# Performance work log

Hardware: AMD Instinct MI355X
Metric: run time of the kernel (lower is better)

The kernel has to match this reference:

```python
import jax, jax.numpy as jnp
import numpy as np

B, D_IN, H, NZ, NC = 32768, 768, 2048, 128, 1024
EPS, NITERS = 0.5, 15


def setup_inputs() -> dict:
    key = jax.random.key(0)
    ks = jax.random.split(key, 4)
    x = jax.random.normal(ks[0], (B, D_IN), jnp.float32)
    # scaled init so feature magnitudes keep exp(-dist/eps) in f32 range
    W1 = jax.random.normal(ks[1], (D_IN, H), jnp.float32) / np.sqrt(D_IN)
    b1 = jnp.zeros((H,), jnp.float32)
    W2 = jax.random.normal(ks[2], (H, NZ), jnp.float32) / np.sqrt(H)
    b2 = jnp.zeros((NZ,), jnp.float32)
    centroids = jax.random.normal(ks[3], (NC, NZ), jnp.float32)
    return {
        'x': x, 'W1': W1, 'b1': b1, 'W2': W2, 'b2': b2,
        'centroids': centroids,
        'cluster_counts': jnp.zeros((NC,), jnp.int32),
        'raw_counts': jnp.zeros((NC,), jnp.int32),
        'total_soft_counts': jnp.zeros((NC,), jnp.float32),
    }


def _sinkhorn(scores, eps=EPS, niters=NITERS):
    # scores: [B, K].  Q: [K, B], matches torch reference where sum(Q) = col-sums.
    Q = jnp.exp(scores / eps).T
    Q = Q / jnp.sum(Q, axis=0, keepdims=True)
    K, Bb = Q.shape
    r = 1.0 / K
    c = 1.0 / Bb

    def body(Q, _):
        Q = Q * (r / jnp.sum(Q, axis=1))[:, None]
        Q = Q * (c / jnp.sum(Q, axis=0))[None, :]
        return Q, None

    Q, _ = jax.lax.scan(body, Q, None, length=niters)
    return (Q / jnp.sum(Q, axis=0, keepdims=True)).T  # [B, K]


def reference(x, W1, b1, W2, b2, centroids, cluster_counts, raw_counts, total_soft_counts):
    # fc backbone: Linear -> ReLU -> Linear
    fv = jax.nn.relu(x @ W1 + b1) @ W2 + b2                        # [B, nz]
    # pairwise euclidean distances to centroids (cdist via gram trick;
    # avoids materializing the [B, nc, nz] broadcast torch creates)
    sq = (jnp.sum(fv * fv, axis=1)[:, None]
          + jnp.sum(centroids * centroids, axis=1)[None, :]
          - 2.0 * fv @ centroids.T)
    cluster_dists = jnp.sqrt(jnp.maximum(sq, 1e-12))               # [B, nc]

    # sinkhorn branch (no_grad in torch)
    soft_assignments = jax.lax.stop_gradient(_sinkhorn(-cluster_dists))
    batch_assignments = jnp.argmin(soft_assignments, axis=1)       # [B]
    soft_counts = jnp.sum(soft_assignments, axis=0)                # [nc]
    # soft_train=False: gather assigned distances
    loss = jnp.mean(jnp.take_along_axis(cluster_dists, batch_assignments[:, None], axis=1))

    # scatter-accumulate counts
    new_raw = raw_counts.at[jnp.argmin(cluster_dists, axis=1)].add(1)
    new_cluster = cluster_counts.at[batch_assignments].add(1)
    new_total_soft = total_soft_counts + soft_counts
    return loss, batch_assignments, soft_counts, new_raw, new_cluster, new_total_soft
```

## Files before the change

### kernel.cpp

```cpp
#include <hip/hip_runtime.h>
#include <math.h>

#define BN    32768
#define DIN   768
#define HN    2048
#define NZ    128
#define NCN   1024

typedef __attribute__((ext_vector_type(8))) short s16x8;
typedef __attribute__((ext_vector_type(4))) float f32x4;
typedef unsigned short u16;

#define MFMA16(a,b,c) __builtin_amdgcn_mfma_f32_16x16x32_bf16(a,b,c,0,0,0)

__device__ __forceinline__ u16 bf16_rne(float x){
  unsigned u = __float_as_uint(x);
  unsigned r = (u + 0x7FFFu + ((u >> 16) & 1u)) >> 16;
  return (u16)r;
}
__device__ __forceinline__ float bf16_tof(u16 h){
  return __uint_as_float(((unsigned)h) << 16);
}
__device__ __forceinline__ void split3(float x, u16& h, u16& m, u16& l){
  h = bf16_rne(x);
  float r1 = x - bf16_tof(h);
  m = bf16_rne(r1);
  float r2 = r1 - bf16_tof(m);
  l = bf16_rne(r2);
}

__device__ __forceinline__ void gload16(const void* gsrc, void* lds){
  __builtin_amdgcn_global_load_lds(
      (const __attribute__((address_space(1))) unsigned int*)gsrc,
      (__attribute__((address_space(3))) unsigned int*)lds, 16, 0, 0);
}

__global__ __launch_bounds__(1024) void k0_init(float* u, int* hraw, int* hclu){
  const int k = threadIdx.x;
  u[k] = 1.0f;
  hraw[k] = 0;
  hclu[k] = 0;
}

__global__ __launch_bounds__(256) void c_split(
    const float* __restrict__ in, u16* __restrict__ oh, u16* __restrict__ om,
    u16* __restrict__ ol, int n4)
{
  const int i = blockIdx.x*256 + threadIdx.x;
  if (i >= n4) return;
  const f32x4 v = *(const f32x4*)&in[(size_t)i*4];
  ushort4 h4, m4, l4;
  split3(v[0], h4.x, m4.x, l4.x);
  split3(v[1], h4.y, m4.y, l4.y);
  split3(v[2], h4.z, m4.z, l4.z);
  split3(v[3], h4.w, m4.w, l4.w);
  *(ushort4*)&oh[(size_t)i*4] = h4;
  *(ushort4*)&om[(size_t)i*4] = m4;
  *(ushort4*)&ol[(size_t)i*4] = l4;
}

__global__ __launch_bounds__(256) void c_tsplit(
    const float* __restrict__ in, int R, int C,
    u16* __restrict__ oh, u16* __restrict__ om, u16* __restrict__ ol)
{
  __shared__ float L[64][65];
  const int t = threadIdx.x;
  const int bi = blockIdx.x, bj = blockIdx.y;
  #pragma unroll
  for (int m=0;m<4;++m){
    int flat = t + 256*m;
    int r = flat >> 4, c4 = (flat & 15) << 2;
    const float4 v = *(const float4*)&in[(size_t)(bi*64 + r)*C + bj*64 + c4];
    L[r][c4+0] = v.x; L[r][c4+1] = v.y; L[r][c4+2] = v.z; L[r][c4+3] = v.w;
  }
  __syncthreads();
  #pragma unroll
  for (int m=0;m<4;++m){
    int flat = t + 256*m;
    int oc = flat >> 4, k4 = (flat & 15) << 2;
    ushort4 h4, m4, l4;
    split3(L[k4+0][oc], h4.x, m4.x, l4.x);
    split3(L[k4+1][oc], h4.y, m4.y, l4.y);
    split3(L[k4+2][oc], h4.z, m4.z, l4.z);
    split3(L[k4+3][oc], h4.w, m4.w, l4.w);
    size_t off = (size_t)(bj*64 + oc)*R + bi*64 + k4;
    *(ushort4*)&oh[off] = h4;
    *(ushort4*)&om[off] = m4;
    *(ushort4*)&ol[off] = l4;
  }
}

__global__ __launch_bounds__(256) void c_norm(
    const float* __restrict__ in, float* __restrict__ out)
{
  const int w = threadIdx.x >> 6, l = threadIdx.x & 63;
  const int row = blockIdx.x*4 + w;
  const float2 v = *(const float2*)&in[(size_t)row*128 + l*2];
  float s = v.x*v.x + v.y*v.y;
  #pragma unroll
  for (int off=32; off; off>>=1) s += __shfl_xor(s, off, 64);
  if (l == 0) out[row] = s;
}

__global__ __launch_bounds__(256, 2) void k1_mfma(
    const u16* __restrict__ Xh, const u16* __restrict__ Xm, const u16* __restrict__ Xl,
    const u16* __restrict__ W1h, const u16* __restrict__ W1m, const u16* __restrict__ W1l,
    const float* __restrict__ b1,
    const u16* __restrict__ W2h, const u16* __restrict__ W2m, const u16* __restrict__ W2l,
    const float* __restrict__ b2, float* __restrict__ fv)
{
  __shared__ __align__(16) unsigned char sm[73728];
  unsigned char* xsr = sm;
  unsigned char* wsr = sm + 24576;

  const int t  = threadIdx.x;
  const int l  = t & 63;
  const int wn = t >> 6;
  const int g  = (l >> 4) & 3;
  const int lr = l & 15;
  const int row0 = blockIdx.x * 64;

  f32x4 fvacc[4][2];
  #pragma unroll
  for (int mf=0;mf<4;++mf){
    fvacc[mf][0] = (f32x4){0.f,0.f,0.f,0.f};
    fvacc[mf][1] = (f32x4){0.f,0.f,0.f,0.f};
  }

  #pragma unroll 1
  for (int g0 = 0; g0 < 8; ++g0){
    f32x4 a1acc[4][4];
    #pragma unroll
    for (int mf=0;mf<4;++mf)
      #pragma unroll
      for (int j=0;j<4;++j) a1acc[mf][j] = (f32x4){0.f,0.f,0.f,0.f};

    #pragma unroll 1
    for (int ks = 0; ks < 12; ++ks){
      #pragma unroll
      for (int i=0;i<6;++i){
        const int ci = wn*6 + i;
        const int s  = ci >> 3;
        const int rb = ci & 7;
        const int xr = rb*8 + (l >> 3);
        const int q  = l & 7;
        const u16* Xp = (s==0) ? Xh : ((s==1) ? Xm : Xl);
        const u16* src = Xp + (size_t)(row0 + xr)*768 + ks*64 + ((q ^ (xr & 7)) << 3);
        gload16(src, xsr + s*8192 + rb*1024);
      }
      #pragma unroll
      for (int sub2=0; sub2<2; ++sub2){
        #pragma unroll
        for (int i=0;i<12;++i){
          const int ci = wn*12 + i;
          const int s  = ci >> 4;
          const int rb = ci & 15;
          const int rloc = rb*8 + (l >> 3);
          const int q  = l & 7;
          const u16* Wp = (s==0) ? W1h : ((s==1) ? W1m : W1l);
          const u16* src = Wp + (size_t)(g0*256 + sub2*128 + rloc)*768 + ks*64
                              + ((q ^ (rloc & 7)) << 3);
          gload16(src, wsr + s*16384 + rb*1024);
        }
        __syncthreads();

        #pragma unroll
        for (int kk=0;kk<2;++kk){
          s16x8 Bf[3][2], Af[3][4];
          #pragma unroll
          for (int s=0;s<3;++s){
            #pragma unroll
            for (int nf=0;nf<2;++nf){
              const int br = wn*32 + nf*16 + lr;
              Bf[s][nf] = *(const s16x8*)(wsr + s*16384 + br*128 + ((16*(g + 4*kk)) ^ ((br & 7) << 4)));
            }
            #pragma unroll
            for (int mf=0;mf<4;++mf){
              const int ar = mf*16 + lr;
              Af[s][mf] = *(const s16x8*)(xsr + s*8192 + ar*128 + ((16*(g + 4*kk)) ^ ((ar & 7) << 4)));
            }
          }
          #pragma unroll
          for (int mf=0;mf<4;++mf){
            #pragma unroll
            for (int nf=0;nf<2;++nf){
              f32x4 acc = a1acc[mf][sub2*2+nf];
              acc = MFMA16(Af[0][mf], Bf[0][nf], acc);
              acc = MFMA16(Af[0][mf], Bf[1][nf], acc);
              acc = MFMA16(Af[1][mf], Bf[0][nf], acc);
              acc = MFMA16(Af[1][mf], Bf[1][nf], acc);
              acc = MFMA16(Af[0][mf], Bf[2][nf], acc);
              acc = MFMA16(Af[2][mf], Bf[0][nf], acc);
              a1acc[mf][sub2*2+nf] = acc;
            }
          }
        }
        __syncthreads();
      }
    }

    float b1v[2][2];
    #pragma unroll
    for (int s2=0;s2<2;++s2)
      #pragma unroll
      for (int nf=0;nf<2;++nf)
        b1v[s2][nf] = b1[g0*256 + s2*128 + wn*32 + nf*16 + lr];

    #pragma unroll
    for (int h=0; h<4; ++h){
      #pragma unroll
      for (int i=0;i<12;++i){
        const int ci = wn*12 + i;
        const int s  = ci >> 4;
        const int rb = ci & 15;
        const int rloc = rb*8 + (l >> 3);
        const int q  = l & 7;
        const u16* Wp = (s==0) ? W2h : ((s==1) ? W2m : W2l);
        const u16* src = Wp + (size_t)rloc*2048 + g0*256 + h*64 + ((q ^ (rloc & 7)) << 3);
        gload16(src, wsr + s*16384 + rb*1024);
      }
      if ((wn >> 1) == (h & 1)){
        #pragma unroll
        for (int mf=0;mf<4;++mf){
          #pragma unroll
          for (int nf=0;nf<2;++nf){
            const int klocal = (wn & 1)*32 + nf*16 + lr;
            #pragma unroll
            for (int r=0;r<4;++r){
              float vv = a1acc[mf][(h>>1)*2+nf][r] + b1v[h>>1][nf];
              vv = vv > 0.f ? vv : 0.f;
              u16 sh, sm2, sl;
              split3(vv, sh, sm2, sl);
              const int ar = mf*16 + g*4 + r;
              const int bo = ar*128 + ((2*klocal) ^ ((ar & 7) << 4));
              *(u16*)(xsr + bo)         = sh;
              *(u16*)(xsr + 8192 + bo)  = sm2;
              *(u16*)(xsr + 16384 + bo) = sl;
            }
          }
        }
      }
      __syncthreads();

      #pragma unroll
      for (int kk=0;kk<2;++kk){
        s16x8 Bf[3][2], Af[3][4];
        #pragma unroll
        for (int s=0;s<3;++s){
          #pragma unroll
          for (int nf=0;nf<2;++nf){
            const int br = wn*32 + nf*16 + lr;
            Bf[s][nf] = *(const s16x8*)(wsr + s*16384 + br*128 + ((16*(g + 4*kk)) ^ ((br & 7) << 4)));
          }
          #pragma unroll
          for (int mf=0;mf<4;++mf){
            const int ar = mf*16 + lr;
            Af[s][mf] = *(const s16x8*)(xsr + s*8192 + ar*128 + ((16*(g + 4*kk)) ^ ((ar & 7) << 4)));
          }
        }
        #pragma unroll
        for (int mf=0;mf<4;++mf){
          #pragma unroll
          for (int nf=0;nf<2;++nf){
            f32x4 acc = fvacc[mf][nf];
            acc = MFMA16(Af[0][mf], Bf[0][nf], acc);
            acc = MFMA16(Af[0][mf], Bf[1][nf], acc);
            acc = MFMA16(Af[1][mf], Bf[0][nf], acc);
            acc = MFMA16(Af[1][mf], Bf[1][nf], acc);
            acc = MFMA16(Af[0][mf], Bf[2][nf], acc);
            acc = MFMA16(Af[2][mf], Bf[0][nf], acc);
            fvacc[mf][nf] = acc;
          }
        }
      }
      __syncthreads();
    }
  }

  const float b2v0 = b2[wn*32 + lr];
  const float b2v1 = b2[wn*32 + 16 + lr];
  #pragma unroll
  for (int mf=0;mf<4;++mf){
    #pragma unroll
    for (int nf=0;nf<2;++nf){
      #pragma unroll
      for (int r=0;r<4;++r){
        const int frow = row0 + mf*16 + g*4 + r;
        const int col  = wn*32 + nf*16 + lr;
        fv[(size_t)frow*NZ + col] = fvacc[mf][nf][r] + ((nf==0) ? b2v0 : b2v1);
      }
    }
  }
}

__global__ __launch_bounds__(256, 2) void k2_mfma(
    const u16* __restrict__ fvh, const u16* __restrict__ fvm, const u16* __restrict__ fvl,
    const u16* __restrict__ ch,  const u16* __restrict__ cm,  const u16* __restrict__ cl,
    const float* __restrict__ fvn, const float* __restrict__ cn,
    float* __restrict__ Q0)
{
  __shared__ __align__(16) unsigned char bs[49152];
  __shared__ float cnl[NCN];
  const int t  = threadIdx.x;
  const int l  = t & 63;
  const int wn = t >> 6;
  const int g  = (l >> 4) & 3;
  const int lr = l & 15;
  const int row0 = blockIdx.x * 64;
  const int arow = row0 + wn*16 + lr;

  s16x8 Af[3][4];
  #pragma unroll
  for (int kk=0;kk<4;++kk){
    const size_t ao = (size_t)arow*128 + kk*32 + g*8;
    Af[0][kk] = *(const s16x8*)&fvh[ao];
    Af[1][kk] = *(const s16x8*)&fvm[ao];
    Af[2][kk] = *(const s16x8*)&fvl[ao];
  }
  #pragma unroll
  for (int m=0;m<4;++m) cnl[t + 256*m] = cn[t + 256*m];
  const f32x4 fvnv = *(const f32x4*)&fvn[row0 + wn*16 + g*4];

  #pragma unroll 1
  for (int cc = 0; cc < NCN; cc += 64){
    #pragma unroll
    for (int i=0;i<12;++i){
      const int ci = wn*12 + i;
      const int s  = ci >> 4;
      const int rb = ci & 15;
      const int crow = rb*4 + (l >> 4);
      const int q  = l & 15;
      const u16* Cp = (s==0) ? ch : ((s==1) ? cm : cl);
      const u16* src = Cp + (size_t)(cc + crow)*128 + ((q ^ (crow & 15)) << 3);
      gload16(src, bs + s*16384 + rb*1024);
    }
    __syncthreads();

    f32x4 acc[4];
    #pragma unroll
    for (int nf=0;nf<4;++nf) acc[nf] = (f32x4){0.f,0.f,0.f,0.f};

    #pragma unroll
    for (int kk=0;kk<4;++kk){
      s16x8 Bq[3][4];
      #pragma unroll
      for (int nf=0;nf<4;++nf){
        const int br = nf*16 + lr;
        const int base = br*256 + (((g + 4*kk) ^ (br & 15)) << 4);
        Bq[0][nf] = *(const s16x8*)(bs + base);
        Bq[1][nf] = *(const s16x8*)(bs + 16384 + base);
        Bq[2][nf] = *(const s16x8*)(bs + 32768 + base);
      }
      #pragma unroll
      for (int nf=0;nf<4;++nf){
        f32x4 a = acc[nf];
        a = MFMA16(Af[0][kk], Bq[0][nf], a);
        a = MFMA16(Af[0][kk], Bq[1][nf], a);
        a = MFMA16(Af[1][kk], Bq[0][nf], a);
        a = MFMA16(Af[1][kk], Bq[1][nf], a);
        a = MFMA16(Af[0][kk], Bq[2][nf], a);
        a = MFMA16(Af[2][kk], Bq[0][nf], a);
        acc[nf] = a;
      }
    }

    #pragma unroll
    for (int nf=0;nf<4;++nf){
      const int n = cc + nf*16 + lr;
      const float cv = cnl[n];
      #pragma unroll
      for (int r=0;r<4;++r){
        float sq = fvnv[r] + cv - 2.0f*acc[nf][r];
        sq = sq > 1e-12f ? sq : 1e-12f;
        const float d = sqrtf(sq);
        Q0[(size_t)(row0 + wn*16 + g*4 + r)*NCN + n] = expf(-2.0f*d);
      }
    }
    __syncthreads();
  }
}

__global__ __launch_bounds__(256) void k3_pass(
    const float* __restrict__ Q0, const float* __restrict__ u,
    float* __restrict__ S_part, float alpha)
{
  __shared__ __align__(16) float Sw[4][NCN];
  const int t = threadIdx.x;
  const int w = t >> 6, l = t & 63;

  f32x4 uu[4], sacc[4];
  #pragma unroll
  for (int j=0;j<4;++j){
    uu[j] = *(const f32x4*)&u[4*(l + 64*j)];
    sacc[j] = (f32x4){0.f,0.f,0.f,0.f};
  }

  const int gw = blockIdx.x*4 + w;
  const size_t b0 = (size_t)gw * 32;
  for (int rr=0; rr<32; ++rr){
    const f32x4* qrow = (const f32x4*)(Q0 + (b0 + rr)*NCN);
    f32x4 q4[4];
    float part = 0.f;
    #pragma unroll
    for (int j=0;j<4;++j){
      q4[j] = qrow[l + 64*j];
      part += q4[j][0]*uu[j][0]; part += q4[j][1]*uu[j][1];
      part += q4[j][2]*uu[j][2]; part += q4[j][3]*uu[j][3];
    }
    #pragma unroll
    for (int off=32; off; off>>=1) part += __shfl_xor(part, off, 64);
    const float v = alpha / part;
    #pragma unroll
    for (int j=0;j<4;++j){
      sacc[j][0] += q4[j][0]*v; sacc[j][1] += q4[j][1]*v;
      sacc[j][2] += q4[j][2]*v; sacc[j][3] += q4[j][3]*v;
    }
  }
  #pragma unroll
  for (int j=0;j<4;++j) *(f32x4*)&Sw[w][4*(l + 64*j)] = sacc[j];
  __syncthreads();
  #pragma unroll
  for (int m=0;m<4;++m){
    int k = t + 256*m;
    S_part[(size_t)blockIdx.x*NCN + k] = ((Sw[0][k]+Sw[1][k])+(Sw[2][k]+Sw[3][k]));
  }
}

__global__ __launch_bounds__(256) void k4_unew(
    const float* __restrict__ S_part, float* __restrict__ u)
{
  __shared__ float P[4][64];
  const int t = threadIdx.x;
  const int col = blockIdx.x*64 + (t & 63);
  const int s4 = t >> 6;
  float p = 0.f;
  for (int i=0;i<64;++i)
    p += S_part[(size_t)(s4*64 + i)*NCN + col];
  P[s4][t & 63] = p;
  __syncthreads();
  if (s4 == 0){
    float tot = ((P[0][t] + P[1][t]) + (P[2][t] + P[3][t]));
    u[col] = (1.0f/1024.0f) / tot;
  }
}

__device__ __forceinline__ float compv(const f32x4 v, int c){
  return (c==0)?v[0]:(c==1)?v[1]:(c==2)?v[2]:v[3];
}

__global__ __launch_bounds__(256) void k5_final(
    const float* __restrict__ Q0, const float* __restrict__ u,
    float* __restrict__ softc_part, float* __restrict__ loss_part,
    int* __restrict__ hist_raw, int* __restrict__ hist_clu,
    float* __restrict__ out_ba)
{
  __shared__ __align__(16) float Sw[4][NCN];
  __shared__ float lossw[4];
  const int t = threadIdx.x;
  const int w = t >> 6, l = t & 63;

  f32x4 uu[4], sacc[4];
  #pragma unroll
  for (int j=0;j<4;++j){
    uu[j] = *(const f32x4*)&u[4*(l + 64*j)];
    sacc[j] = (f32x4){0.f,0.f,0.f,0.f};
  }

  const int gw = blockIdx.x*4 + w;
  const size_t b0 = (size_t)gw * 32;
  float lacc = 0.f;
  for (int rr=0; rr<32; ++rr){
    const size_t b = b0 + rr;
    const f32x4* qrow = (const f32x4*)(Q0 + b*NCN);
    f32x4 q4[4], wv4[4];
    float part = 0.f;
    #pragma unroll
    for (int j=0;j<4;++j){
      q4[j] = qrow[l + 64*j];
      wv4[j][0] = uu[j][0]*q4[j][0]; wv4[j][1] = uu[j][1]*q4[j][1];
      wv4[j][2] = uu[j][2]*q4[j][2]; wv4[j][3] = uu[j][3]*q4[j][3];
      part += wv4[j][0]; part += wv4[j][1]; part += wv4[j][2]; part += wv4[j][3];
    }
    #pragma unroll
    for (int off=32; off; off>>=1) part += __shfl_xor(part, off, 64);
    const float inv = 1.0f / part;

    float smin = wv4[0][0] * inv; int kmin = 4*l; float qat = q4[0][0];
    float qmax = q4[0][0];        int kmax = 4*l;
    #pragma unroll
    for (int j=0;j<4;++j){
      #pragma unroll
      for (int c=0;c<4;++c){
        if (j==0 && c==0) continue;
        float qv = compv(q4[j], c);
        float sv = compv(wv4[j], c) * inv;
        int k = 4*l + 256*j + c;
        if (sv < smin){ smin = sv; kmin = k; qat = qv; }
        if (qv > qmax){ qmax = qv; kmax = k; }
      }
    }
    #pragma unroll
    for (int off=32; off; off>>=1){
      float s2 = __shfl_xor(smin, off, 64);
      int   k2 = __shfl_xor(kmin, off, 64);
      float q2 = __shfl_xor(qat,  off, 64);
      if (s2 < smin || (s2 == smin && k2 < kmin)){ smin=s2; kmin=k2; qat=q2; }
      float m2 = __shfl_xor(qmax, off, 64);
      int   i2 = __shfl_xor(kmax, off, 64);
      if (m2 > qmax || (m2 == qmax && i2 < kmax)){ qmax=m2; kmax=i2; }
    }
    #pragma unroll
    for (int j=0;j<4;++j){
      sacc[j][0] += wv4[j][0]*inv; sacc[j][1] += wv4[j][1]*inv;
      sacc[j][2] += wv4[j][2]*inv; sacc[j][3] += wv4[j][3]*inv;
    }
    if (l == 0){
      out_ba[b] = (float)kmin;
      atomicAdd(&hist_clu[kmin], 1);
      atomicAdd(&hist_raw[kmax], 1);
      lacc += -0.5f * logf(qat);
    }
  }
  #pragma unroll
  for (int j=0;j<4;++j) *(f32x4*)&Sw[w][4*(l + 64*j)] = sacc[j];
  if (l == 0) lossw[w] = lacc;
  __syncthreads();
  #pragma unroll
  for (int m=0;m<4;++m){
    int k = t + 256*m;
    softc_part[(size_t)blockIdx.x*NCN + k] = ((Sw[0][k]+Sw[1][k])+(Sw[2][k]+Sw[3][k]));
  }
  if (t == 0) loss_part[blockIdx.x] = ((lossw[0]+lossw[1])+(lossw[2]+lossw[3]));
}

__global__ __launch_bounds__(1024) void k6_fin(
    const float* __restrict__ softc_part, const float* __restrict__ loss_part,
    const int* __restrict__ hist_raw, const int* __restrict__ hist_clu,
    const int* __restrict__ raw_in, const int* __restrict__ clu_in,
    const float* __restrict__ tsoft_in, float* __restrict__ out)
{
  const int k = threadIdx.x;
  float s0=0.f,s1=0.f,s2=0.f,s3=0.f;
  for (int blk=0; blk<256; blk+=4){
    s0 += softc_part[(size_t)(blk+0)*NCN + k];
    s1 += softc_part[(size_t)(blk+1)*NCN + k];
    s2 += softc_part[(size_t)(blk+2)*NCN + k];
    s3 += softc_part[(size_t)(blk+3)*NCN + k];
  }
  const float s = ((s0+s1)+(s2+s3));
  out[1 + BN + k]           = s;
  out[1 + BN + NCN + k]     = (float)(raw_in[k] + hist_raw[k]);
  out[1 + BN + 2*NCN + k]   = (float)(clu_in[k] + hist_clu[k]);
  out[1 + BN + 3*NCN + k]   = tsoft_in[k] + s;
  if (k == 0){
    float ls = 0.f;
    for (int i=0;i<256;++i) ls += loss_part[i];
    out[0] = ls / 32768.0f;
  }
}

extern "C" void kernel_launch(void* const* d_in, const int* in_sizes, int n_in,
                              void* d_out, int out_size, void* d_ws, size_t ws_size,
                              hipStream_t stream) {
  (void)in_sizes; (void)n_in; (void)out_size; (void)ws_size;
  const float* x      = (const float*)d_in[0];
  const float* W1     = (const float*)d_in[1];
  const float* b1     = (const float*)d_in[2];
  const float* W2     = (const float*)d_in[3];
  const float* b2     = (const float*)d_in[4];
  const float* cent   = (const float*)d_in[5];
  const int*   clu_in = (const int*)d_in[6];
  const int*   raw_in = (const int*)d_in[7];
  const float* tsoft  = (const float*)d_in[8];
  float* out = (float*)d_out;

  float* ws        = (float*)d_ws;
  float* fv        = ws;
  float* Q0        = ws + 4194304;
  u16*   Xh        = (u16*)Q0;
  u16*   Xm        = Xh + 25165824;
  u16*   Xl        = Xm + 25165824;
  float* u         = ws + 41943040;
  float* S_part    = u + 1024;
  float* softc_par = S_part + 524288;
  float* loss_par  = softc_par + 262144;
  int*   hist_raw  = (int*)(loss_par + 256);
  int*   hist_clu  = hist_raw + 1024;
  float* wbase     = (float*)(hist_clu + 1024);
  u16* W1Th = (u16*)wbase;
  u16* W1Tm = W1Th + 1572864;
  u16* W1Tl = W1Tm + 1572864;
  u16* W2Th = W1Tl + 1572864;
  u16* W2Tm = W2Th + 262144;
  u16* W2Tl = W2Tm + 262144;
  u16* fvh = (u16*)wbase;
  u16* fvm = fvh + 4194304;
  u16* fvl = fvm + 4194304;
  u16* ch  = fvl + 4194304;
  u16* cm  = ch  + 131072;
  u16* cl  = cm  + 131072;
  float* fvn = wbase + 6488064;
  float* cn  = fvn + 32768;

  c_split <<<24576, 256, 0, stream>>>(x, Xh, Xm, Xl, 6291456);
  c_tsplit<<<dim3(12, 32), 256, 0, stream>>>(W1, 768, 2048, W1Th, W1Tm, W1Tl);
  c_tsplit<<<dim3(32, 2),  256, 0, stream>>>(W2, 2048, 128, W2Th, W2Tm, W2Tl);
  k0_init<<<1, 1024, 0, stream>>>(u, hist_raw, hist_clu);

  k1_mfma<<<512, 256, 0, stream>>>(Xh, Xm, Xl, W1Th, W1Tm, W1Tl, b1,
                                   W2Th, W2Tm, W2Tl, b2, fv);

  c_split<<<4096, 256, 0, stream>>>(fv,   fvh, fvm, fvl, 1048576);
  c_split<<<128,  256, 0, stream>>>(cent, ch,  cm,  cl,  32768);
  c_norm <<<8192, 256, 0, stream>>>(fv,   fvn);
  c_norm <<<256,  256, 0, stream>>>(cent, cn);

  k2_mfma<<<512, 256, 0, stream>>>(fvh, fvm, fvl, ch, cm, cl, fvn, cn, Q0);

  for (int it = 0; it < 15; ++it){
    const float alpha = (it == 0) ? 1.0f : (1.0f/32768.0f);
    k3_pass<<<256, 256, 0, stream>>>(Q0, u, S_part, alpha);
    k4_unew<<<16, 256, 0, stream>>>(S_part, u);
  }
  k5_final<<<256, 256, 0, stream>>>(Q0, u, softc_par, loss_par,
                                    hist_raw, hist_clu, out + 1);
  k6_fin<<<1, 1024, 0, stream>>>(softc_par, loss_par, hist_raw, hist_clu,
                                 raw_in, clu_in, tsoft, out);
}
```

Before: 1.454 ms.

## Restructure fused MLP chunking, swizzle blocks, and widen Sinkhorn pass grids

The fused MLP kernel now processes the hidden dimension in 128-wide chunks instead of 256, halving the first-layer accumulator registers, and it issues the W2 tile load after the ReLU/split write. Block indices in k1 and k2 are swizzled so that neighbouring blocks handle spread-out rows. The Sinkhorn row pass and the final kernel launch twice as many blocks with 16 rows per wave, and the row pass batches four rows so their shuffle reductions interleave. The column-reduction kernel uses 64 blocks with a tree reduction, and the workspace layout is moved to hold the larger partial-sum arrays. The aim is more parallelism and occupancy in the memory-bound Sinkhorn loop and lower register pressure in the GEMM, in exchange for more partial sums to reduce and more W1 re-streaming.

```diff
diff --git a/kernel.cpp b/kernel.cpp
--- a/kernel.cpp
+++ b/kernel.cpp
@@ -118,7 +118,9 @@
   const int wn = t >> 6;
   const int g  = (l >> 4) & 3;
   const int lr = l & 15;
-  const int row0 = blockIdx.x * 64;
+  const int bid = blockIdx.x;
+  const int swz = (bid & 7)*64 + (bid >> 3);
+  const int row0 = swz * 64;
 
   f32x4 fvacc[4][2];
   #pragma unroll
@@ -128,12 +130,13 @@
   }
 
   #pragma unroll 1
-  for (int g0 = 0; g0 < 8; ++g0){
-    f32x4 a1acc[4][4];
-    #pragma unroll
-    for (int mf=0;mf<4;++mf)
-      #pragma unroll
-      for (int j=0;j<4;++j) a1acc[mf][j] = (f32x4){0.f,0.f,0.f,0.f};
+  for (int nc = 0; nc < 16; ++nc){
+    f32x4 a1acc[4][2];
+    #pragma unroll
+    for (int mf=0;mf<4;++mf){
+      a1acc[mf][0] = (f32x4){0.f,0.f,0.f,0.f};
+      a1acc[mf][1] = (f32x4){0.f,0.f,0.f,0.f};
+    }
 
     #pragma unroll 1
     for (int ks = 0; ks < 12; ++ks){
@@ -149,77 +152,58 @@
         gload16(src, xsr + s*8192 + rb*1024);
       }
       #pragma unroll
-      for (int sub2=0; sub2<2; ++sub2){
-        #pragma unroll
-        for (int i=0;i<12;++i){
-          const int ci = wn*12 + i;
-          const int s  = ci >> 4;
-          const int rb = ci & 15;
-          const int rloc = rb*8 + (l >> 3);
-          const int q  = l & 7;
-          const u16* Wp = (s==0) ? W1h : ((s==1) ? W1m : W1l);
-          const u16* src = Wp + (size_t)(g0*256 + sub2*128 + rloc)*768 + ks*64
-                              + ((q ^ (rloc & 7)) << 3);
-          gload16(src, wsr + s*16384 + rb*1024);
-        }
-        __syncthreads();
-
-        #pragma unroll
-        for (int kk=0;kk<2;++kk){
-          s16x8 Bf[3][2], Af[3][4];
-          #pragma unroll
-          for (int s=0;s<3;++s){
-            #pragma unroll
-            for (int nf=0;nf<2;++nf){
-              const int br = wn*32 + nf*16 + lr;
-              Bf[s][nf] = *(const s16x8*)(wsr + s*16384 + br*128 + ((16*(g + 4*kk)) ^ ((br & 7) << 4)));
-            }
-            #pragma unroll
-            for (int mf=0;mf<4;++mf){
-              const int ar = mf*16 + lr;
-              Af[s][mf] = *(const s16x8*)(xsr + s*8192 + ar*128 + ((16*(g + 4*kk)) ^ ((ar & 7) << 4)));
-            }
-          }
-          #pragma unroll
-          for (int mf=0;mf<4;++mf){
-            #pragma unroll
-            for (int nf=0;nf<2;++nf){
-              f32x4 acc = a1acc[mf][sub2*2+nf];
-              acc = MFMA16(Af[0][mf], Bf[0][nf], acc);
-              acc = MFMA16(Af[0][mf], Bf[1][nf], acc);
-              acc = MFMA16(Af[1][mf], Bf[0][nf], acc);
-              acc = MFMA16(Af[1][mf], Bf[1][nf], acc);
-              acc = MFMA16(Af[0][mf], Bf[2][nf], acc);
-              acc = MFMA16(Af[2][mf], Bf[0][nf], acc);
-              a1acc[mf][sub2*2+nf] = acc;
-            }
-          }
-        }
-        __syncthreads();
-      }
-    }
-
-    float b1v[2][2];
-    #pragma unroll
-    for (int s2=0;s2<2;++s2)
-      #pragma unroll
-      for (int nf=0;nf<2;++nf)
-        b1v[s2][nf] = b1[g0*256 + s2*128 + wn*32 + nf*16 + lr];
-
-    #pragma unroll
-    for (int h=0; h<4; ++h){
-      #pragma unroll
       for (int i=0;i<12;++i){
         const int ci = wn*12 + i;
         const int s  = ci >> 4;
         const int rb = ci & 15;
         const int rloc = rb*8 + (l >> 3);
         const int q  = l & 7;
-        const u16* Wp = (s==0) ? W2h : ((s==1) ? W2m : W2l);
-        const u16* src = Wp + (size_t)rloc*2048 + g0*256 + h*64 + ((q ^ (rloc & 7)) << 3);
+        const u16* Wp = (s==0) ? W1h : ((s==1) ? W1m : W1l);
+        const u16* src = Wp + (size_t)(nc*128 + rloc)*768 + ks*64 + ((q ^ (rloc & 7)) << 3);
         gload16(src, wsr + s*16384 + rb*1024);
       }
-      if ((wn >> 1) == (h & 1)){
+      __syncthreads();
+
+      #pragma unroll
+      for (int kk=0;kk<2;++kk){
+        s16x8 Bf[3][2], Af[3][4];
+        #pragma unroll
+        for (int s=0;s<3;++s){
+          #pragma unroll
+          for (int nf=0;nf<2;++nf){
+            const int br = wn*32 + nf*16 + lr;
+            Bf[s][nf] = *(const s16x8*)(wsr + s*16384 + br*128 + ((16*(g + 4*kk)) ^ ((br & 7) << 4)));
+          }
+          #pragma unroll
+          for (int mf=0;mf<4;++mf){
+            const int ar = mf*16 + lr;
+            Af[s][mf] = *(const s16x8*)(xsr + s*8192 + ar*128 + ((16*(g + 4*kk)) ^ ((ar & 7) << 4)));
+          }
+        }
+        #pragma unroll
+        for (int mf=0;mf<4;++mf){
+          #pragma unroll
+          for (int nf=0;nf<2;++nf){
+            f32x4 acc = a1acc[mf][nf];
+            acc = MFMA16(Af[0][mf], Bf[0][nf], acc);
+            acc = MFMA16(Af[0][mf], Bf[1][nf], acc);
+            acc = MFMA16(Af[1][mf], Bf[0][nf], acc);
+            acc = MFMA16(Af[1][mf], Bf[1][nf], acc);
+            acc = MFMA16(Af[0][mf], Bf[2][nf], acc);
+            acc = MFMA16(Af[2][mf], Bf[0][nf], acc);
+            a1acc[mf][nf] = acc;
+          }
+        }
+      }
+      __syncthreads();
+    }
+
+    const float b1v0 = b1[nc*128 + wn*32 + lr];
+    const float b1v1 = b1[nc*128 + wn*32 + 16 + lr];
+
+    #pragma unroll
+    for (int half=0; half<2; ++half){
+      if ((wn >> 1) == half){
         #pragma unroll
         for (int mf=0;mf<4;++mf){
           #pragma unroll
@@ -227,7 +211,7 @@
             const int klocal = (wn & 1)*32 + nf*16 + lr;
             #pragma unroll
             for (int r=0;r<4;++r){
-              float vv = a1acc[mf][(h>>1)*2+nf][r] + b1v[h>>1][nf];
+              float vv = a1acc[mf][nf][r] + ((nf==0) ? b1v0 : b1v1);
               vv = vv > 0.f ? vv : 0.f;
               u16 sh, sm2, sl;
               split3(vv, sh, sm2, sl);
@@ -239,6 +223,17 @@
             }
           }
         }
+      }
+      #pragma unroll
+      for (int i=0;i<12;++i){
+        const int ci = wn*12 + i;
+        const int s  = ci >> 4;
+        const int rb = ci & 15;
+        const int rloc = rb*8 + (l >> 3);
+        const int q  = l & 7;
+        const u16* Wp = (s==0) ? W2h : ((s==1) ? W2m : W2l);
+        const u16* src = Wp + (size_t)rloc*2048 + nc*128 + half*64 + ((q ^ (rloc & 7)) << 3);
+        gload16(src, wsr + s*16384 + rb*1024);
       }
       __syncthreads();
 
@@ -306,7 +301,9 @@
   const int wn = t >> 6;
   const int g  = (l >> 4) & 3;
   const int lr = l & 15;
-  const int row0 = blockIdx.x * 64;
+  const int bid = blockIdx.x;
+  const int swz = (bid & 7)*64 + (bid >> 3);
+  const int row0 = swz * 64;
   const int arow = row0 + wn*16 + lr;
 
   s16x8 Af[3][4];
@@ -380,7 +377,7 @@
   }
 }
 
-__global__ __launch_bounds__(256) void k3_pass(
+__global__ __launch_bounds__(256, 2) void k3_pass(
     const float* __restrict__ Q0, const float* __restrict__ u,
     float* __restrict__ S_part, float alpha)
 {
@@ -396,24 +393,36 @@
   }
 
   const int gw = blockIdx.x*4 + w;
-  const size_t b0 = (size_t)gw * 32;
-  for (int rr=0; rr<32; ++rr){
-    const f32x4* qrow = (const f32x4*)(Q0 + (b0 + rr)*NCN);
-    f32x4 q4[4];
-    float part = 0.f;
-    #pragma unroll
-    for (int j=0;j<4;++j){
-      q4[j] = qrow[l + 64*j];
-      part += q4[j][0]*uu[j][0]; part += q4[j][1]*uu[j][1];
-      part += q4[j][2]*uu[j][2]; part += q4[j][3]*uu[j][3];
-    }
-    #pragma unroll
-    for (int off=32; off; off>>=1) part += __shfl_xor(part, off, 64);
-    const float v = alpha / part;
-    #pragma unroll
-    for (int j=0;j<4;++j){
-      sacc[j][0] += q4[j][0]*v; sacc[j][1] += q4[j][1]*v;
-      sacc[j][2] += q4[j][2]*v; sacc[j][3] += q4[j][3]*v;
+  const size_t b0 = (size_t)gw * 16;
+  #pragma unroll 1
+  for (int rr=0; rr<16; rr+=4){
+    f32x4 q[4][4];
+    float part[4];
+    #pragma unroll
+    for (int rq=0;rq<4;++rq){
+      const f32x4* qrow = (const f32x4*)(Q0 + (b0 + rr + rq)*NCN);
+      float p = 0.f;
+      #pragma unroll
+      for (int j=0;j<4;++j){
+        q[rq][j] = qrow[l + 64*j];
+        p += q[rq][j][0]*uu[j][0]; p += q[rq][j][1]*uu[j][1];
+        p += q[rq][j][2]*uu[j][2]; p += q[rq][j][3]*uu[j][3];
+      }
+      part[rq] = p;
+    }
+    #pragma unroll
+    for (int off=32; off; off>>=1){
+      #pragma unroll
+      for (int rq=0;rq<4;++rq) part[rq] += __shfl_xor(part[rq], off, 64);
+    }
+    #pragma unroll
+    for (int rq=0;rq<4;++rq){
+      const float v = alpha / part[rq];
+      #pragma unroll
+      for (int j=0;j<4;++j){
+        sacc[j][0] += q[rq][j][0]*v; sacc[j][1] += q[rq][j][1]*v;
+        sacc[j][2] += q[rq][j][2]*v; sacc[j][3] += q[rq][j][3]*v;
+      }
     }
   }
   #pragma unroll
@@ -429,26 +438,26 @@
 __global__ __launch_bounds__(256) void k4_unew(
     const float* __restrict__ S_part, float* __restrict__ u)
 {
-  __shared__ float P[4][64];
+  __shared__ float P[256];
   const int t = threadIdx.x;
-  const int col = blockIdx.x*64 + (t & 63);
-  const int s4 = t >> 6;
+  const int c = t & 15;
+  const int seg = t >> 4;
+  const int col = blockIdx.x*16 + c;
   float p = 0.f;
-  for (int i=0;i<64;++i)
-    p += S_part[(size_t)(s4*64 + i)*NCN + col];
-  P[s4][t & 63] = p;
+  #pragma unroll 4
+  for (int i=0;i<32;++i)
+    p += S_part[(size_t)(seg*32 + i)*NCN + col];
+  P[seg*16 + c] = p;
   __syncthreads();
-  if (s4 == 0){
-    float tot = ((P[0][t] + P[1][t]) + (P[2][t] + P[3][t]));
-    u[col] = (1.0f/1024.0f) / tot;
-  }
-}
-
-__device__ __forceinline__ float compv(const f32x4 v, int c){
-  return (c==0)?v[0]:(c==1)?v[1]:(c==2)?v[2]:v[3];
-}
-
-__global__ __launch_bounds__(256) void k5_final(
+  #pragma unroll
+  for (int s2=8; s2>0; s2>>=1){
+    if (seg < s2) P[seg*16 + c] += P[(seg+s2)*16 + c];
+    __syncthreads();
+  }
+  if (seg == 0) u[col] = (1.0f/1024.0f) / P[c];
+}
+
+__global__ __launch_bounds__(256, 2) void k5_final(
     const float* __restrict__ Q0, const float* __restrict__ u,
     float* __restrict__ softc_part, float* __restrict__ loss_part,
     int* __restrict__ hist_raw, int* __restrict__ hist_clu,
@@ -467,9 +476,10 @@
   }
 
   const int gw = blockIdx.x*4 + w;
-  const size_t b0 = (size_t)gw * 32;
+  const size_t b0 = (size_t)gw * 16;
   float lacc = 0.f;
-  for (int rr=0; rr<32; ++rr){
+  #pragma unroll 1
+  for (int rr=0; rr<16; ++rr){
     const size_t b = b0 + rr;
     const f32x4* qrow = (const f32x4*)(Q0 + b*NCN);
     f32x4 q4[4], wv4[4];
@@ -492,9 +502,9 @@
       #pragma unroll
       for (int c=0;c<4;++c){
         if (j==0 && c==0) continue;
-        float qv = compv(q4[j], c);
-        float sv = compv(wv4[j], c) * inv;
-        int k = 4*l + 256*j + c;
+        const float qv = q4[j][c];
+        const float sv = wv4[j][c] * inv;
+        const int k = 4*(l + 64*j) + c;
         if (sv < smin){ smin = sv; kmin = k; qat = qv; }
         if (qv > qmax){ qmax = qv; kmax = k; }
       }
@@ -541,7 +551,7 @@
 {
   const int k = threadIdx.x;
   float s0=0.f,s1=0.f,s2=0.f,s3=0.f;
-  for (int blk=0; blk<256; blk+=4){
+  for (int blk=0; blk<512; blk+=4){
     s0 += softc_part[(size_t)(blk+0)*NCN + k];
     s1 += softc_part[(size_t)(blk+1)*NCN + k];
     s2 += softc_part[(size_t)(blk+2)*NCN + k];
@@ -554,7 +564,7 @@
   out[1 + BN + 3*NCN + k]   = tsoft_in[k] + s;
   if (k == 0){
     float ls = 0.f;
-    for (int i=0;i<256;++i) ls += loss_part[i];
+    for (int i=0;i<512;++i) ls += loss_part[i];
     out[0] = ls / 32768.0f;
   }
 }
@@ -580,11 +590,11 @@
   u16*   Xh        = (u16*)Q0;
   u16*   Xm        = Xh + 25165824;
   u16*   Xl        = Xm + 25165824;
+  float* softc_par = ws + 37748736;
+  float* loss_par  = softc_par + 524288;
   float* u         = ws + 41943040;
   float* S_part    = u + 1024;
-  float* softc_par = S_part + 524288;
-  float* loss_par  = softc_par + 262144;
-  int*   hist_raw  = (int*)(loss_par + 256);
+  int*   hist_raw  = (int*)(S_part + 524288);
   int*   hist_clu  = hist_raw + 1024;
   float* wbase     = (float*)(hist_clu + 1024);
   u16* W1Th = (u16*)wbase;
@@ -601,6 +611,7 @@
   u16* cl  = cm  + 131072;
   float* fvn = wbase + 6488064;
   float* cn  = fvn + 32768;
+  float* out_ba = out + 1;
 
   c_split <<<24576, 256, 0, stream>>>(x, Xh, Xm, Xl, 6291456);
   c_tsplit<<<dim3(12, 32), 256, 0, stream>>>(W1, 768, 2048, W1Th, W1Tm, W1Tl);
@@ -619,11 +630,11 @@
 
   for (int it = 0; it < 15; ++it){
     const float alpha = (it == 0) ? 1.0f : (1.0f/32768.0f);
-    k3_pass<<<256, 256, 0, stream>>>(Q0, u, S_part, alpha);
-    k4_unew<<<16, 256, 0, stream>>>(S_part, u);
-  }
-  k5_final<<<256, 256, 0, stream>>>(Q0, u, softc_par, loss_par,
-                                    hist_raw, hist_clu, out + 1);
+    k3_pass<<<512, 256, 0, stream>>>(Q0, u, S_part, alpha);
+    k4_unew<<<64, 256, 0, stream>>>(S_part, u);
+  }
+  k5_final<<<512, 256, 0, stream>>>(Q0, u, softc_par, loss_par,
+                                    hist_raw, hist_clu, out_ba);
   k6_fin<<<1, 1024, 0, stream>>>(softc_par, loss_par, hist_raw, hist_clu,
                                  raw_in, clu_in, tsoft, out);
 }
```

New measurement: 1.283 ms. -11.7%, faster.
